# Optimization experiments

Hardware: AMD Instinct MI355X
Metric: run time of the kernel (lower is better)

The kernel has to match this reference:

```python
import jax, jax.numpy as jnp
import numpy as np

B, S, D = 2, 2048, 2048
H, HKV = 32, 8
DH = D // H          # 64
G = H // HKV         # group size 4


def setup_inputs() -> dict:
    key = jax.random.key(0)
    ks = jax.random.split(key, 5)
    sc = lambda fan_in: 1.0 / np.sqrt(fan_in)
    return {
        "hidden_states": jax.random.normal(ks[0], (B, S, D), jnp.float32),
        "Wq": jax.random.normal(ks[1], (D, D), jnp.float32) * sc(D),
        "bq": jnp.zeros((D,), jnp.float32),
        "Wk": jax.random.normal(ks[2], (D, HKV * DH), jnp.float32) * sc(D),
        "bk": jnp.zeros((HKV * DH,), jnp.float32),
        "Wv": jax.random.normal(ks[3], (D, HKV * DH), jnp.float32) * sc(D),
        "bv": jnp.zeros((HKV * DH,), jnp.float32),
        "Wo": jax.random.normal(ks[4], (D, D), jnp.float32) * sc(D),
        "bo": jnp.zeros((D,), jnp.float32),
    }


def reference(hidden_states, Wq, bq, Wk, bk, Wv, bv, Wo, bo):
    x = hidden_states
    # projections
    q = x @ Wq + bq                     # [B,S,D]
    k = x @ Wk + bk                     # [B,S,HKV*DH]
    v = x @ Wv + bv
    # split heads; group queries so K/V broadcast instead of repeat_interleave
    # (same math: repeat_interleave expands kv head j to query heads j*G..j*G+G-1)
    q = q.reshape(B, S, HKV, G, DH).transpose(0, 2, 3, 1, 4)  # [B,HKV,G,S,DH]
    k = k.reshape(B, S, HKV, DH).transpose(0, 2, 1, 3)        # [B,HKV,S,DH]
    v = v.reshape(B, S, HKV, DH).transpose(0, 2, 1, 3)
    scale = 1.0 / jnp.sqrt(jnp.asarray(DH, q.dtype))
    scores = jnp.einsum('bhgqd,bhkd->bhgqk', q, k) * scale    # [B,HKV,G,S,S]
    attn = jax.nn.softmax(scores, axis=-1)
    ctx = jnp.einsum('bhgqk,bhkd->bhgqd', attn, v)            # [B,HKV,G,S,DH]
    # merge heads back to [B,S,D] (head order = kv_head*G + group idx)
    merged = ctx.transpose(0, 3, 1, 2, 4).reshape(B, S, D)
    out = merged @ Wo + bo
    return out
```

## Files before the change

### kernel.cpp

```cpp
#include <hip/hip_runtime.h>
#include <cstdint>

typedef __bf16 bf16;
typedef __attribute__((ext_vector_type(8))) __bf16 bf16x8;
typedef __attribute__((ext_vector_type(4))) __bf16 bf16x4;
typedef __attribute__((ext_vector_type(4))) float f32x4;

#define B_   2
#define S_   2048
#define D_   2048
#define HKV_ 8
#define H_   32
#define DH_  64

__device__ __forceinline__ void async_cp16(const bf16* g, bf16* l) {
  __builtin_amdgcn_global_load_lds(
      (__attribute__((address_space(1))) void*)g,
      (__attribute__((address_space(3))) void*)l,
      16, 0, 0);
}

__global__ __launch_bounds__(256) void transpose_k(
    const float* __restrict__ in, bf16* __restrict__ out, int R, int C) {
  __shared__ bf16 tile[64][65];
  const int tx = threadIdx.x & 63;
  const int ty = threadIdx.x >> 6;
  const int r0 = blockIdx.x * 64;
  const int c0 = blockIdx.y * 64;
#pragma unroll
  for (int j = 0; j < 16; ++j) {
    int r = j * 4 + ty;
    tile[r][tx] = (bf16)in[(size_t)(r0 + r) * C + c0 + tx];
  }
  __syncthreads();
#pragma unroll
  for (int j = 0; j < 16; ++j) {
    int r = j * 4 + ty;
    out[(size_t)(c0 + r) * R + r0 + tx] = tile[tx][r];
  }
}

template <typename AT, int OMODE>
__global__ __launch_bounds__(256) void gemm_bt(
    const AT* __restrict__ A, const bf16* __restrict__ Bt,
    const float* __restrict__ b1, const float* __restrict__ b2,
    const float* __restrict__ b3,
    void* __restrict__ C0, void* __restrict__ C1, void* __restrict__ C2,
    int N, int K) {
  __shared__ bf16 a_tile[128 * 64];
  __shared__ bf16 b_tile[128 * 64];
  const int tid  = threadIdx.x;
  const int wave = tid >> 6;
  const int lane = tid & 63;
  const int quad = lane >> 4;
  const int l16  = lane & 15;
  const int m0   = blockIdx.x * 128;
  const int n0   = blockIdx.y * 128;
  const int wm   = (wave >> 1) * 64;
  const int wn   = (wave & 1) * 64;

  f32x4 acc[4][4] = {};

  const int srow  = wave * 32 + (lane >> 3);
  const int skoff = (lane & 7) * 8;
  const AT*   Ag = A  + (size_t)(m0 + srow) * K + skoff;
  const bf16* Bg = Bt + (size_t)(n0 + srow) * K + skoff;
  bf16* al = &a_tile[srow * 64 + skoff];
  bf16* bl = &b_tile[srow * 64 + skoff];

  for (int kt = 0; kt < K; kt += 64) {
    bf16x8 areg[4];
    if constexpr (sizeof(AT) == 4) {
#pragma unroll
      for (int c = 0; c < 4; ++c) {
        const float* ap = (const float*)(Ag + (size_t)(c * 8) * K + kt);
        float4 lo = *(const float4*)ap;
        float4 hi = *(const float4*)(ap + 4);
        areg[c][0] = (bf16)lo.x; areg[c][1] = (bf16)lo.y;
        areg[c][2] = (bf16)lo.z; areg[c][3] = (bf16)lo.w;
        areg[c][4] = (bf16)hi.x; areg[c][5] = (bf16)hi.y;
        areg[c][6] = (bf16)hi.z; areg[c][7] = (bf16)hi.w;
      }
    }
    __syncthreads();
    if constexpr (sizeof(AT) == 4) {
#pragma unroll
      for (int c = 0; c < 4; ++c) *(bf16x8*)(al + c * 512) = areg[c];
    } else {
#pragma unroll
      for (int c = 0; c < 4; ++c)
        async_cp16((const bf16*)Ag + (size_t)(c * 8) * K + kt, al + c * 512);
    }
#pragma unroll
    for (int c = 0; c < 4; ++c)
      async_cp16(Bg + (size_t)(c * 8) * K + kt, bl + c * 512);
    __syncthreads();
#pragma unroll
    for (int kk = 0; kk < 64; kk += 32) {
      bf16x8 af[4], bfr[4];
#pragma unroll
      for (int i = 0; i < 4; ++i) {
        af[i]  = *(const bf16x8*)&a_tile[(wm + i * 16 + l16) * 64 + kk + quad * 8];
        bfr[i] = *(const bf16x8*)&b_tile[(wn + i * 16 + l16) * 64 + kk + quad * 8];
      }
#pragma unroll
      for (int i = 0; i < 4; ++i)
#pragma unroll
        for (int j = 0; j < 4; ++j)
          acc[i][j] = __builtin_amdgcn_mfma_f32_16x16x32_bf16(af[i], bfr[j], acc[i][j], 0, 0, 0);
    }
  }

#pragma unroll
  for (int i = 0; i < 4; ++i) {
    const int row = m0 + wm + i * 16 + quad * 4;
#pragma unroll
    for (int j = 0; j < 4; ++j) {
      const int col = n0 + wn + j * 16 + l16;
      if constexpr (OMODE == 2) {
        const float bia = b1[col];
#pragma unroll
        for (int r = 0; r < 4; ++r)
          ((float*)C0)[(size_t)(row + r) * N + col] = acc[i][j][r] + bia;
      } else {
        if (col < 2048) {
          const float bia = b1[col];
#pragma unroll
          for (int r = 0; r < 4; ++r)
            ((bf16*)C0)[(size_t)(row + r) * 2048 + col] = (bf16)((acc[i][j][r] + bia) * 0.125f);
        } else if (col < 2560) {
          const int cc = col - 2048;
          const float bia = b2[cc];
#pragma unroll
          for (int r = 0; r < 4; ++r)
            ((bf16*)C1)[(size_t)(row + r) * 512 + cc] = (bf16)(acc[i][j][r] + bia);
        } else {
          const int cc = col - 2560;
          const float bia = b3[cc];
          const int hh = cc >> 6, dd = cc & 63;
#pragma unroll
          for (int r = 0; r < 4; ++r) {
            const int rr = row + r;
            const int bb = rr >> 11, ss = rr & 2047;
            ((bf16*)C2)[((((size_t)bb * HKV_ + hh) * DH_ + dd) << 11) + ss] =
                (bf16)(acc[i][j][r] + bia);
          }
        }
      }
    }
  }
}

__global__ __launch_bounds__(256) void gqa_flash(
    const bf16* __restrict__ Qs,
    const bf16* __restrict__ Kb,
    const bf16* __restrict__ VT,
    bf16* __restrict__ ctx) {
  __shared__ bf16 k_tile[128 * 72];
  __shared__ bf16 vt_tile[64 * 136];
  __shared__ bf16 p_tile[4][16 * 136];

  const int tid  = threadIdx.x;
  const int wave = tid >> 6;
  const int lane = tid & 63;
  const int quad = lane >> 4;
  const int l16  = lane & 15;

  const int qt = blockIdx.x;
  const int hq = blockIdx.y;
  const int b  = blockIdx.z;
  const int h  = hq >> 2;

  bf16x8 qf[2][2];
  const int qrow0 = b * S_ + qt * 128 + wave * 32;
#pragma unroll
  for (int im = 0; im < 2; ++im)
#pragma unroll
    for (int kk = 0; kk < 2; ++kk)
      qf[im][kk] = *(const bf16x8*)&Qs[(size_t)(qrow0 + im * 16 + l16) * D_ +
                                       hq * DH_ + kk * 32 + quad * 8];

  f32x4 o_acc[2][4] = {};
  float l_run[2] = {0.f, 0.f};

  const int srow  = wave * 32 + (lane >> 3);
  const int skoff = (lane & 7) * 8;
  const int vrow  = wave * 16 + (lane >> 4);
  const int vkoff = (lane & 15) * 8;
  const bf16* Kg = Kb + (size_t)(b * S_ + srow) * (HKV_ * DH_) + h * DH_ + skoff;
  const bf16* Vg = VT + ((size_t)(b * HKV_ + h) * DH_ + vrow) * S_ + vkoff;
  bf16* kl = &k_tile[srow * 72 + skoff];
  bf16* vl = &vt_tile[vrow * 136 + vkoff];
  bf16* pw = &p_tile[wave][l16 * 136];

  bf16x8 kreg[4], vreg[4];
#pragma unroll
  for (int c = 0; c < 4; ++c) {
    kreg[c] = *(const bf16x8*)(Kg + (size_t)(c * 8) * (HKV_ * DH_));
    vreg[c] = *(const bf16x8*)(Vg + (size_t)(c * 4) * S_);
  }

  for (int kt = 0; kt < S_; kt += 128) {
    __syncthreads();
#pragma unroll
    for (int c = 0; c < 4; ++c) {
      *(bf16x8*)(kl + c * 8 * 72)  = kreg[c];
      *(bf16x8*)(vl + c * 4 * 136) = vreg[c];
    }
    __syncthreads();

    if (kt + 128 < S_) {
      const int ktn = kt + 128;
#pragma unroll
      for (int c = 0; c < 4; ++c) {
        kreg[c] = *(const bf16x8*)(Kg + (size_t)(ktn + c * 8) * (HKV_ * DH_));
        vreg[c] = *(const bf16x8*)(Vg + (size_t)(c * 4) * S_ + ktn);
      }
    }

#pragma unroll
    for (int im = 0; im < 2; ++im) {
      f32x4 st[8] = {};
#pragma unroll
      for (int kk = 0; kk < 2; ++kk)
#pragma unroll
        for (int in = 0; in < 8; ++in) {
          bf16x8 ak = *(const bf16x8*)&k_tile[(in * 16 + l16) * 72 + kk * 32 + quad * 8];
          st[in] = __builtin_amdgcn_mfma_f32_16x16x32_bf16(ak, qf[im][kk], st[in], 0, 0, 0);
        }

      float sm = 0.f;
#pragma unroll
      for (int in = 0; in < 8; ++in) {
        bf16x4 pv;
#pragma unroll
        for (int r = 0; r < 4; ++r) {
          float p = __expf(st[in][r]);
          sm += p;
          pv[r] = (bf16)p;
        }
        *(bf16x4*)(pw + in * 16 + quad * 4) = pv;
      }
      sm += __shfl_xor(sm, 16);
      sm += __shfl_xor(sm, 32);
      l_run[im] += sm;

#pragma unroll
      for (int kq = 0; kq < 4; ++kq) {
        bf16x8 pb = *(const bf16x8*)(pw + kq * 32 + quad * 8);
#pragma unroll
        for (int jm = 0; jm < 4; ++jm) {
          bf16x8 av = *(const bf16x8*)&vt_tile[(jm * 16 + l16) * 136 + kq * 32 + quad * 8];
          o_acc[im][jm] = __builtin_amdgcn_mfma_f32_16x16x32_bf16(av, pb, o_acc[im][jm], 0, 0, 0);
        }
      }
    }
  }

#pragma unroll
  for (int im = 0; im < 2; ++im) {
    const float inv_l = 1.f / l_run[im];
    const size_t row = (size_t)(qrow0 + im * 16 + l16);
#pragma unroll
    for (int jm = 0; jm < 4; ++jm) {
      bf16x4 ov;
#pragma unroll
      for (int r = 0; r < 4; ++r) ov[r] = (bf16)(o_acc[im][jm][r] * inv_l);
      *(bf16x4*)&ctx[row * D_ + hq * DH_ + jm * 16 + quad * 4] = ov;
    }
  }
}

extern "C" void kernel_launch(void* const* d_in, const int* in_sizes, int n_in,
                              void* d_out, int out_size, void* d_ws, size_t ws_size,
                              hipStream_t stream) {
  const float* x  = (const float*)d_in[0];
  const float* Wq = (const float*)d_in[1];
  const float* bq = (const float*)d_in[2];
  const float* Wk = (const float*)d_in[3];
  const float* bk = (const float*)d_in[4];
  const float* Wv = (const float*)d_in[5];
  const float* bv = (const float*)d_in[6];
  const float* Wo = (const float*)d_in[7];
  const float* bo = (const float*)d_in[8];
  float* out = (float*)d_out;

  char* ws = (char*)d_ws;
  bf16* WT  = (bf16*)(ws);
  bf16* ctx = (bf16*)(ws);
  bf16* WoT = (bf16*)(ws + 16777216);
  bf16* Qs  = (bf16*)(ws + 25165824);
  bf16* Kb  = (bf16*)(ws + 41943040);
  bf16* VT  = (bf16*)(ws + 46137344);

  dim3 blk(256);
  transpose_k<<<dim3(32, 32), blk, 0, stream>>>(Wq, WT, 2048, 2048);
  transpose_k<<<dim3(32, 8),  blk, 0, stream>>>(Wk, WT + (size_t)2048 * 2048, 2048, 512);
  transpose_k<<<dim3(32, 8),  blk, 0, stream>>>(Wv, WT + (size_t)2560 * 2048, 2048, 512);
  transpose_k<<<dim3(32, 32), blk, 0, stream>>>(Wo, WoT, 2048, 2048);

  gemm_bt<float, 3><<<dim3(32, 24), blk, 0, stream>>>(
      x, WT, bq, bk, bv, Qs, Kb, VT, 3072, 2048);

  gqa_flash<<<dim3(16, 32, 2), blk, 0, stream>>>(Qs, Kb, VT, ctx);

  gemm_bt<bf16, 2><<<dim3(32, 16), blk, 0, stream>>>(
      ctx, WoT, bo, nullptr, nullptr, out, nullptr, nullptr, 2048, 2048);
}
```

Measured before the change: 368.5 us.

## Switch attention to 32x32x16 MFMA with register-resident P via permlane32 swap

The flash attention kernel moves from 16x16x32 MFMA tiles to 32x32x16 tiles. The softmax probabilities are repacked into the B-operand layout with permlane32_swap instead of a round trip through per-wave shared memory. The padded K and V^T shared tiles become unpadded XOR-swizzled layouts, which removes the P tile and the padding from LDS. This cuts LDS traffic and instruction count per tile, but relies on the exact lane mapping of the swizzle and permlane being correct.

```diff
diff --git a/kernel.cpp b/kernel.cpp
--- a/kernel.cpp
+++ b/kernel.cpp
@@ -4,7 +4,9 @@
 typedef __bf16 bf16;
 typedef __attribute__((ext_vector_type(8))) __bf16 bf16x8;
 typedef __attribute__((ext_vector_type(4))) __bf16 bf16x4;
+typedef __attribute__((ext_vector_type(2))) __bf16 bf16x2;
 typedef __attribute__((ext_vector_type(4))) float f32x4;
+typedef __attribute__((ext_vector_type(16))) float f32x16;
 
 #define B_   2
 #define S_   2048
@@ -156,42 +158,36 @@
     const bf16* __restrict__ Kb,
     const bf16* __restrict__ VT,
     bf16* __restrict__ ctx) {
-  __shared__ bf16 k_tile[128 * 72];
-  __shared__ bf16 vt_tile[64 * 136];
-  __shared__ bf16 p_tile[4][16 * 136];
+  __shared__ bf16 k_tile[128 * 64];
+  __shared__ bf16 vt_tile[64 * 128];
 
   const int tid  = threadIdx.x;
   const int wave = tid >> 6;
   const int lane = tid & 63;
-  const int quad = lane >> 4;
-  const int l16  = lane & 15;
+  const int l32  = lane & 31;
+  const int hi   = lane >> 5;
 
   const int qt = blockIdx.x;
   const int hq = blockIdx.y;
   const int b  = blockIdx.z;
   const int h  = hq >> 2;
 
-  bf16x8 qf[2][2];
+  bf16x8 qf[4];
   const int qrow0 = b * S_ + qt * 128 + wave * 32;
 #pragma unroll
-  for (int im = 0; im < 2; ++im)
-#pragma unroll
-    for (int kk = 0; kk < 2; ++kk)
-      qf[im][kk] = *(const bf16x8*)&Qs[(size_t)(qrow0 + im * 16 + l16) * D_ +
-                                       hq * DH_ + kk * 32 + quad * 8];
-
-  f32x4 o_acc[2][4] = {};
-  float l_run[2] = {0.f, 0.f};
+  for (int ks = 0; ks < 4; ++ks)
+    qf[ks] = *(const bf16x8*)&Qs[(size_t)(qrow0 + l32) * D_ +
+                                 hq * DH_ + ks * 16 + hi * 8];
+
+  f32x16 o_acc[2] = {};
+  float l_run = 0.f;
 
   const int srow  = wave * 32 + (lane >> 3);
-  const int skoff = (lane & 7) * 8;
+  const int kgran = (lane & 7) ^ ((lane >> 3) & 7);
   const int vrow  = wave * 16 + (lane >> 4);
-  const int vkoff = (lane & 15) * 8;
-  const bf16* Kg = Kb + (size_t)(b * S_ + srow) * (HKV_ * DH_) + h * DH_ + skoff;
-  const bf16* Vg = VT + ((size_t)(b * HKV_ + h) * DH_ + vrow) * S_ + vkoff;
-  bf16* kl = &k_tile[srow * 72 + skoff];
-  bf16* vl = &vt_tile[vrow * 136 + vkoff];
-  bf16* pw = &p_tile[wave][l16 * 136];
+  const bf16* Kg = Kb + (size_t)(b * S_ + srow) * (HKV_ * DH_) + h * DH_ + (lane & 7) * 8;
+  const bf16* Vg = VT + ((size_t)(b * HKV_ + h) * DH_ + vrow) * S_ + (lane & 15) * 8;
+  bf16* kl = &k_tile[srow * 64 + kgran * 8];
 
   bf16x8 kreg[4], vreg[4];
 #pragma unroll
@@ -204,8 +200,10 @@
     __syncthreads();
 #pragma unroll
     for (int c = 0; c < 4; ++c) {
-      *(bf16x8*)(kl + c * 8 * 72)  = kreg[c];
-      *(bf16x8*)(vl + c * 4 * 136) = vreg[c];
+      *(bf16x8*)(kl + c * 8 * 64) = kreg[c];
+      const int row = vrow + 4 * c;
+      const int g = (lane & 15) ^ (row & 7);
+      *(bf16x8*)&vt_tile[row * 128 + g * 8] = vreg[c];
     }
     __syncthreads();
 
@@ -219,56 +217,65 @@
     }
 
 #pragma unroll
-    for (int im = 0; im < 2; ++im) {
-      f32x4 st[8] = {};
-#pragma unroll
-      for (int kk = 0; kk < 2; ++kk)
-#pragma unroll
-        for (int in = 0; in < 8; ++in) {
-          bf16x8 ak = *(const bf16x8*)&k_tile[(in * 16 + l16) * 72 + kk * 32 + quad * 8];
-          st[in] = __builtin_amdgcn_mfma_f32_16x16x32_bf16(ak, qf[im][kk], st[in], 0, 0, 0);
+    for (int kb = 0; kb < 4; ++kb) {
+      f32x16 st = {};
+#pragma unroll
+      for (int ks = 0; ks < 4; ++ks) {
+        const int krow = kb * 32 + l32;
+        const int g = (ks * 2 + hi) ^ (krow & 7);
+        bf16x8 kf = *(const bf16x8*)&k_tile[krow * 64 + g * 8];
+        st = __builtin_amdgcn_mfma_f32_32x32x16_bf16(kf, qf[ks], st, 0, 0, 0);
+      }
+
+      float sm = 0.f;
+      int w[4][2];
+#pragma unroll
+      for (int j = 0; j < 4; ++j)
+#pragma unroll
+        for (int pp = 0; pp < 2; ++pp) {
+          const float p0 = __expf(st[4 * j + 2 * pp]);
+          const float p1 = __expf(st[4 * j + 2 * pp + 1]);
+          sm += p0 + p1;
+          bf16x2 t; t[0] = (bf16)p0; t[1] = (bf16)p1;
+          w[j][pp] = __builtin_bit_cast(int, t);
         }
-
-      float sm = 0.f;
-#pragma unroll
-      for (int in = 0; in < 8; ++in) {
-        bf16x4 pv;
-#pragma unroll
-        for (int r = 0; r < 4; ++r) {
-          float p = __expf(st[in][r]);
-          sm += p;
-          pv[r] = (bf16)p;
+      l_run += sm;
+
+#pragma unroll
+      for (int kqlo = 0; kqlo < 2; ++kqlo) {
+        auto r0 = __builtin_amdgcn_permlane32_swap(
+            w[2 * kqlo][0], w[2 * kqlo + 1][0], false, false);
+        auto r1 = __builtin_amdgcn_permlane32_swap(
+            w[2 * kqlo][1], w[2 * kqlo + 1][1], false, false);
+        union { int wi[4]; bf16x8 v; } pb;
+        pb.wi[0] = r0[0]; pb.wi[1] = r1[0];
+        pb.wi[2] = r0[1]; pb.wi[3] = r1[1];
+        const int kq = kb * 2 + kqlo;
+#pragma unroll
+        for (int jm = 0; jm < 2; ++jm) {
+          const int vr = jm * 32 + l32;
+          const int g = (kq * 2 + hi) ^ (vr & 7);
+          bf16x8 av = *(const bf16x8*)&vt_tile[vr * 128 + g * 8];
+          o_acc[jm] = __builtin_amdgcn_mfma_f32_32x32x16_bf16(av, pb.v, o_acc[jm], 0, 0, 0);
         }
-        *(bf16x4*)(pw + in * 16 + quad * 4) = pv;
-      }
-      sm += __shfl_xor(sm, 16);
-      sm += __shfl_xor(sm, 32);
-      l_run[im] += sm;
-
-#pragma unroll
-      for (int kq = 0; kq < 4; ++kq) {
-        bf16x8 pb = *(const bf16x8*)(pw + kq * 32 + quad * 8);
-#pragma unroll
-        for (int jm = 0; jm < 4; ++jm) {
-          bf16x8 av = *(const bf16x8*)&vt_tile[(jm * 16 + l16) * 136 + kq * 32 + quad * 8];
-          o_acc[im][jm] = __builtin_amdgcn_mfma_f32_16x16x32_bf16(av, pb, o_acc[im][jm], 0, 0, 0);
-        }
-      }
-    }
-  }
-
-#pragma unroll
-  for (int im = 0; im < 2; ++im) {
-    const float inv_l = 1.f / l_run[im];
-    const size_t row = (size_t)(qrow0 + im * 16 + l16);
-#pragma unroll
-    for (int jm = 0; jm < 4; ++jm) {
+      }
+    }
+  }
+
+  l_run += __shfl_xor(l_run, 32);
+  const float inv_l = 1.f / l_run;
+
+  const size_t qrow = (size_t)(qrow0 + l32);
+#pragma unroll
+  for (int jm = 0; jm < 2; ++jm)
+#pragma unroll
+    for (int c = 0; c < 4; ++c) {
       bf16x4 ov;
 #pragma unroll
-      for (int r = 0; r < 4; ++r) ov[r] = (bf16)(o_acc[im][jm][r] * inv_l);
-      *(bf16x4*)&ctx[row * D_ + hq * DH_ + jm * 16 + quad * 4] = ov;
-    }
-  }
+      for (int j = 0; j < 4; ++j) ov[j] = (bf16)(o_acc[jm][4 * c + j] * inv_l);
+      const int dh0 = jm * 32 + c * 8 + hi * 4;
+      *(bf16x4*)&ctx[qrow * D_ + hq * DH_ + dh0] = ov;
+    }
 }
 
 extern "C" void kernel_launch(void* const* d_in, const int* in_sizes, int n_in,
```

After: 331.4 us. 10.1% less time.
